# Optimization experiments

Hardware: AMD Instinct MI355X
Metric: run time of the kernel (lower is better)

## Reference

```python
import jax, jax.numpy as jnp
import numpy as np


def setup_inputs() -> dict:
    key = jax.random.key(0)
    k1, k2 = jax.random.split(key)
    bsz, beam_size, step, n = 256, 4, 511, 3
    R = bsz * beam_size          # 1024 hypothesis rows
    L = step + 1                 # 512 tokens generated so far
    V = 50257                    # vocab size
    tokens = jax.random.randint(k1, (R, L), 0, 100, dtype=jnp.int64)
    lprobs = jax.random.normal(k2, (R, V), dtype=jnp.float32)
    return {
        "tokens": tokens,
        "lprobs": lprobs,
        "bsz": bsz,
        "step": step,
        "beam_size": beam_size,
        "no_repeat_ngram_size": n,
    }


def reference(tokens, lprobs, bsz, step, beam_size, no_repeat_ngram_size):
    """Block repeated n-grams: for every row (hypothesis), find all earlier
    (n-1)-grams equal to the trailing (n-1) tokens and set lprobs of the
    token that followed each match to -inf (same math as the CUDA kernel)."""
    n = no_repeat_ngram_size  # static Python int
    R, V = lprobs.shape
    if step + 2 - n <= 0:
        return lprobs  # not enough history yet; kernel is a no-op
    K = step - n + 2                      # number of candidate n-gram starts
    last = tokens[:, step - n + 2:step + 1]           # [R, n-1] trailing context
    starts = jnp.arange(K)
    win_idx = starts[:, None] + jnp.arange(n - 1)[None, :]  # [K, n-1]
    windows = tokens[:, win_idx]                      # [R, K, n-1]
    banned = tokens[:, starts + n - 1]                # [R, K] token after each n-gram
    match = jnp.all(windows == last[:, None, :], axis=-1)   # [R, K]
    rows = jnp.arange(R)[:, None]
    mask = jnp.zeros((R, V), dtype=bool).at[rows, banned].max(match)  # scatter-or
    return jnp.where(mask, -jnp.inf, lprobs)
```

## Files before the change

kernel.cpp:

```cpp
#include <hip/hip_runtime.h>
#include <math.h>

#define NEG_BIG (-3.0e38f)

__global__ void ngram_copy_kernel(const float* __restrict__ in,
                                  float* __restrict__ out,
                                  long long n_elems) {
    long long nvec = n_elems >> 2;
    long long i = (long long)blockIdx.x * blockDim.x + threadIdx.x;
    if (i < nvec) {
        float4 v = ((const float4*)in)[i];
        ((float4*)out)[i] = v;
    }
    long long tail = n_elems & 3LL;
    if (blockIdx.x == 0 && (long long)threadIdx.x < tail) {
        long long idx = (nvec << 2) + threadIdx.x;
        out[idx] = in[idx];
    }
}

__global__ void ngram_scatter_kernel(const void* __restrict__ tokens_raw,
                                     float* __restrict__ out,
                                     const int* __restrict__ p_bsz,
                                     const int* __restrict__ p_step,
                                     const int* __restrict__ p_beam,
                                     const int* __restrict__ p_n,
                                     long long out_elems) {
    const int bsz  = *p_bsz;
    const int step = *p_step;
    const int beam = *p_beam;
    const int n    = *p_n;

    const int R = bsz * beam;
    const int L = step + 1;
    const long long V = out_elems / R;
    const int K = step - n + 2;
    if (K <= 0) return;

    const int* t32 = (const int*)tokens_raw;
    bool is64 = true;
    int probe = (2 * L < 256) ? 2 * L : 256;
    for (int i = 1; i < probe; i += 2) {
        if (t32[i] != 0) { is64 = false; break; }
    }
    const long long* t64 = (const long long*)tokens_raw;

    const int last_base = step - n + 2;

    for (int row = blockIdx.x; row < R; row += gridDim.x) {
        const long long rb = (long long)row * L;
        for (int k = threadIdx.x; k < K; k += blockDim.x) {
            bool match = true;
            for (int j = 0; j < n - 1; ++j) {
                int a = is64 ? (int)t64[rb + k + j]        : t32[rb + k + j];
                int b = is64 ? (int)t64[rb + last_base + j] : t32[rb + last_base + j];
                match = match && (a == b);
            }
            if (match) {
                int banned = is64 ? (int)t64[rb + k + n - 1] : t32[rb + k + n - 1];
                if (banned >= 0 && banned < (int)V) {
                    out[(long long)row * V + banned] = NEG_BIG;
                }
            }
        }
    }
}

extern "C" void kernel_launch(void* const* d_in, const int* in_sizes, int n_in,
                              void* d_out, int out_size, void* d_ws, size_t ws_size,
                              hipStream_t stream) {
    const void*  tokens = d_in[0];
    const float* lprobs = (const float*)d_in[1];
    const int*   p_bsz  = (const int*)d_in[2];
    const int*   p_step = (const int*)d_in[3];
    const int*   p_beam = (const int*)d_in[4];
    const int*   p_n    = (const int*)d_in[5];
    float* out = (float*)d_out;

    long long n_elems = (long long)out_size;
    long long nvec = n_elems >> 2;
    int threads = 256;
    long long blocks = (nvec + threads - 1) / threads;
    if (blocks < 1) blocks = 1;

    ngram_copy_kernel<<<(dim3)(unsigned)blocks, threads, 0, stream>>>(lprobs, out, n_elems);

    ngram_scatter_kernel<<<1024, 256, 0, stream>>>(tokens, out, p_bsz, p_step,
                                                   p_beam, p_n, n_elems);
}
```

Measured before the change: 343.3 us.

## Fuse copy and n-gram scatter into one row-segmented kernel

Replaces the separate full-array copy kernel and the scatter kernel with a single kernel. Each block copies one quarter of a row with nontemporal vector loads and stores, then applies the n-gram bans that fall inside that segment. This removes a second launch and the dependency between the two passes, and the dtype probe now uses a wavefront ballot instead of a serial loop. The cost is that every segment re-runs the token match over the whole row (four times per row), and each block adds two barriers.

```diff
diff --git a/kernel.cpp b/kernel.cpp
--- a/kernel.cpp
+++ b/kernel.cpp
@@ -3,29 +3,20 @@
 
 #define NEG_BIG (-3.0e38f)
 
-__global__ void ngram_copy_kernel(const float* __restrict__ in,
-                                  float* __restrict__ out,
-                                  long long n_elems) {
-    long long nvec = n_elems >> 2;
-    long long i = (long long)blockIdx.x * blockDim.x + threadIdx.x;
-    if (i < nvec) {
-        float4 v = ((const float4*)in)[i];
-        ((float4*)out)[i] = v;
-    }
-    long long tail = n_elems & 3LL;
-    if (blockIdx.x == 0 && (long long)threadIdx.x < tail) {
-        long long idx = (nvec << 2) + threadIdx.x;
-        out[idx] = in[idx];
-    }
-}
+#define SEGS 4
 
-__global__ void ngram_scatter_kernel(const void* __restrict__ tokens_raw,
-                                     float* __restrict__ out,
-                                     const int* __restrict__ p_bsz,
-                                     const int* __restrict__ p_step,
-                                     const int* __restrict__ p_beam,
-                                     const int* __restrict__ p_n,
-                                     long long out_elems) {
+typedef float v4f __attribute__((ext_vector_type(4)));
+
+__global__ __launch_bounds__(256) void ngram_fused_kernel(
+    const void* __restrict__ tokens_raw,
+    const float* __restrict__ in,
+    float*       __restrict__ out,
+    const int*   __restrict__ p_bsz,
+    const int*   __restrict__ p_step,
+    const int*   __restrict__ p_beam,
+    const int*   __restrict__ p_n,
+    long long out_elems)
+{
     const int bsz  = *p_bsz;
     const int step = *p_step;
     const int beam = *p_beam;
@@ -35,33 +26,65 @@
     const int L = step + 1;
     const long long V = out_elems / R;
     const int K = step - n + 2;
-    if (K <= 0) return;
-
-    const int* t32 = (const int*)tokens_raw;
-    bool is64 = true;
-    int probe = (2 * L < 256) ? 2 * L : 256;
-    for (int i = 1; i < probe; i += 2) {
-        if (t32[i] != 0) { is64 = false; break; }
-    }
-    const long long* t64 = (const long long*)tokens_raw;
-
     const int last_base = step - n + 2;
 
-    for (int row = blockIdx.x; row < R; row += gridDim.x) {
-        const long long rb = (long long)row * L;
-        for (int k = threadIdx.x; k < K; k += blockDim.x) {
-            bool match = true;
-            for (int j = 0; j < n - 1; ++j) {
-                int a = is64 ? (int)t64[rb + k + j]        : t32[rb + k + j];
-                int b = is64 ? (int)t64[rb + last_base + j] : t32[rb + last_base + j];
-                match = match && (a == b);
+    const int*       t32 = (const int*)tokens_raw;
+    const long long* t64 = (const long long*)tokens_raw;
+    const int lane = threadIdx.x & 63;
+    const int probe_i = (lane < L) ? (2 * lane + 1) : 1;
+    const bool odd_nonzero = (t32[probe_i] != 0);
+    const bool is64 = (__ballot(odd_nonzero) == 0ULL);
+
+    const int tid = threadIdx.x;
+    const int nthreads = blockDim.x;
+
+    const long long seg_len = (V + SEGS - 1) / SEGS;
+    const long long total_work = (long long)R * SEGS;
+
+    for (long long work = blockIdx.x; work < total_work; work += gridDim.x) {
+        const int row = (int)(work / SEGS);
+        const int seg = (int)(work % SEGS);
+        const long long s0 = (long long)seg * seg_len;
+        long long s1 = s0 + seg_len; if (s1 > V) s1 = V;
+        if (s0 >= s1) continue;
+        const long long rowbase = (long long)row * V;
+
+        const long long g0 = rowbase + s0;
+        const long long g1 = rowbase + s1;
+        long long ga = (g0 + 3) & ~3LL; if (ga > g1) ga = g1;
+        long long gv = g1 & ~3LL;       if (gv < ga) gv = ga;
+
+        if (tid < (int)(ga - g0)) out[g0 + tid] = in[g0 + tid];
+        {
+            const v4f* iv = (const v4f*)(in + ga);
+            v4f*       ov = (v4f*)(out + ga);
+            const long long nv = (gv - ga) >> 2;
+            for (long long i = tid; i < nv; i += nthreads) {
+                v4f v = __builtin_nontemporal_load(&iv[i]);
+                __builtin_nontemporal_store(v, &ov[i]);
             }
-            if (match) {
-                int banned = is64 ? (int)t64[rb + k + n - 1] : t32[rb + k + n - 1];
-                if (banned >= 0 && banned < (int)V) {
-                    out[(long long)row * V + banned] = NEG_BIG;
+        }
+        if (tid < (int)(g1 - gv)) out[gv + tid] = in[gv + tid];
+
+        if (K > 0) {
+            __syncthreads();
+            const long long rb = (long long)row * L;
+            for (int k = tid; k < K; k += nthreads) {
+                bool match = true;
+                for (int j = 0; j < n - 1; ++j) {
+                    const int a = is64 ? (int)t64[rb + k + j]         : t32[rb + k + j];
+                    const int b = is64 ? (int)t64[rb + last_base + j] : t32[rb + last_base + j];
+                    match = match && (a == b);
+                }
+                if (match) {
+                    const long long banned =
+                        is64 ? (long long)t64[rb + k + n - 1] : (long long)t32[rb + k + n - 1];
+                    if (banned >= s0 && banned < s1) {
+                        out[rowbase + banned] = NEG_BIG;
+                    }
                 }
             }
+            __syncthreads();
         }
     }
 }
@@ -77,14 +100,7 @@
     const int*   p_n    = (const int*)d_in[5];
     float* out = (float*)d_out;
 
-    long long n_elems = (long long)out_size;
-    long long nvec = n_elems >> 2;
-    int threads = 256;
-    long long blocks = (nvec + threads - 1) / threads;
-    if (blocks < 1) blocks = 1;
-
-    ngram_copy_kernel<<<(dim3)(unsigned)blocks, threads, 0, stream>>>(lprobs, out, n_elems);
-
-    ngram_scatter_kernel<<<1024, 256, 0, stream>>>(tokens, out, p_bsz, p_step,
-                                                   p_beam, p_n, n_elems);
+    ngram_fused_kernel<<<4096, 256, 0, stream>>>(tokens, lprobs, out,
+                                                 p_bsz, p_step, p_beam, p_n,
+                                                 (long long)out_size);
 }
```

Measured after the change: 359.5 us. 1.05x slower.
